# Kernel optimization log

Hardware: AMD Instinct MI355X
Metric: run time of the kernel (lower is better)

Reference implementation:

```python
import jax, jax.numpy as jnp
import numpy as np

NUM_GRAPHS = 64
NEG_SLOPE = 0.2


def _gatv2_layer(x, src, dst, edge_attr, Wl, Wr, We, att, b):
    """PyG GATv2Conv (heads=1) with self-loops (fill_value='mean')."""
    n = x.shape[0]
    # self-loop edge_attr = mean of incoming edge_attr per target node
    ones = jnp.ones((src.shape[0],), dtype=x.dtype)
    deg = jax.ops.segment_sum(ones, dst, num_segments=n)
    ea_sum = jax.ops.segment_sum(edge_attr, dst, num_segments=n)
    loop_attr = ea_sum / jnp.maximum(deg, 1.0)[:, None]
    loop = jnp.arange(n)
    src_f = jnp.concatenate([src, loop])
    dst_f = jnp.concatenate([dst, loop])
    ea_f = jnp.concatenate([edge_attr, loop_attr], axis=0)

    xl = x @ Wl              # source transform [N, out]
    xr = x @ Wr              # target transform [N, out]
    ee = ea_f @ We           # edge transform   [E+N, out]

    m = xl[src_f] + xr[dst_f] + ee                      # [E+N, out]
    m = jax.nn.leaky_relu(m, NEG_SLOPE)
    s = m @ att                                         # [E+N] attention logits

    # segment softmax over incoming edges of each target node
    smax = jax.ops.segment_max(s, dst_f, num_segments=n)
    e = jnp.exp(s - smax[dst_f])
    denom = jax.ops.segment_sum(e, dst_f, num_segments=n)
    alpha = e / (denom[dst_f] + 1e-16)

    out = jax.ops.segment_sum(alpha[:, None] * xl[src_f], dst_f, num_segments=n)
    return out + b


def setup_inputs() -> dict:
    key = jax.random.key(0)
    ks = jax.random.split(key, 16)
    N, E, D, ED = 50000, 640000, 128, 16
    sc = 0.1
    inp = {
        "node_features": jax.random.normal(ks[0], (N, D), jnp.float32),
        "edge_index": jax.random.randint(ks[1], (2, E), 0, N, jnp.int64),
        "batch": jnp.sort(jax.random.randint(ks[2], (N,), 0, 64, jnp.int64)),
        "edge_attr": jax.random.normal(ks[3], (E, ED), jnp.float32),
        "Wl1": jax.random.normal(ks[4], (D, D), jnp.float32) * sc,
        "Wr1": jax.random.normal(ks[5], (D, D), jnp.float32) * sc,
        "We1": jax.random.normal(ks[6], (ED, D), jnp.float32) * sc,
        "att1": jax.random.normal(ks[7], (D,), jnp.float32) * sc,
        "b1": jnp.zeros((D,), jnp.float32),
        "Wl2": jax.random.normal(ks[8], (D, D), jnp.float32) * sc,
        "Wr2": jax.random.normal(ks[9], (D, D), jnp.float32) * sc,
        "We2": jax.random.normal(ks[10], (ED, D), jnp.float32) * sc,
        "att2": jax.random.normal(ks[11], (D,), jnp.float32) * sc,
        "b2": jnp.zeros((D,), jnp.float32),
    }
    return inp


def reference(node_features, edge_index, batch, edge_attr,
              Wl1, Wr1, We1, att1, b1, Wl2, Wr2, We2, att2, b2):
    src, dst = edge_index[0], edge_index[1]
    x = _gatv2_layer(node_features, src, dst, edge_attr, Wl1, Wr1, We1, att1, b1)
    x = jax.nn.relu(x)
    x = _gatv2_layer(x, src, dst, edge_attr, Wl2, Wr2, We2, att2, b2)
    x = jax.nn.relu(x)
    # global mean pool over the full node set (node_subset_indices defaults to arange)
    cnt = jax.ops.segment_sum(jnp.ones((x.shape[0],), x.dtype), batch, num_segments=NUM_GRAPHS)
    pooled = jax.ops.segment_sum(x, batch, num_segments=NUM_GRAPHS)
    return pooled / jnp.maximum(cnt, 1.0)[:, None]
```

## Files before the change

### kernel.cpp

```cpp
#include <hip/hip_runtime.h>
#include <hip/hip_bf16.h>
#include <math.h>

#define D 128
#define ED 16
#define NUM_GRAPHS 64
#define SCAN_CHUNK 2048


__global__ void deg_kernel(const int* __restrict__ dst, int* __restrict__ deg, int E) {
  int e = blockIdx.x * 256 + threadIdx.x;
  if (e < E) atomicAdd(&deg[dst[e]], 1);
}

__global__ __launch_bounds__(256) void scan_reduce_kernel(const int* __restrict__ deg,
                                                          int* __restrict__ bsum, int N) {
  int b = blockIdx.x, tid = threadIdx.x;
  int base = b * SCAN_CHUNK + tid * 8;
  int s = 0;
#pragma unroll
  for (int j = 0; j < 8; ++j) {
    int idx = base + j;
    if (idx < N) s += deg[idx];
  }
#pragma unroll
  for (int off = 1; off < 64; off <<= 1) s += __shfl_xor(s, off);
  __shared__ int ws[4];
  int lane = tid & 63, w = tid >> 6;
  if (lane == 0) ws[w] = s;
  __syncthreads();
  if (tid == 0) bsum[b] = ws[0] + ws[1] + ws[2] + ws[3];
}

__global__ void scan_bsum_kernel(const int* __restrict__ bsum, int* __restrict__ boff,
                                 int* __restrict__ rowptrN, int B) {
  int tid = threadIdx.x;
  int v = (tid < B) ? bsum[tid] : 0;
  int x = v;
#pragma unroll
  for (int off = 1; off < 64; off <<= 1) {
    int y = __shfl_up(x, off);
    if (tid >= off) x += y;
  }
  if (tid < B) boff[tid] = x - v;
  if (tid == 63) *rowptrN = x;
}

__global__ __launch_bounds__(256) void scan_write_kernel(const int* __restrict__ deg,
                                                         const int* __restrict__ boff,
                                                         int* __restrict__ rowptr, int N) {
  int b = blockIdx.x, tid = threadIdx.x;
  int lane = tid & 63, w = tid >> 6;
  int base = b * SCAN_CHUNK + tid * 8;
  int v[8];
  int s = 0;
#pragma unroll
  for (int j = 0; j < 8; ++j) {
    int idx = base + j;
    v[j] = (idx < N) ? deg[idx] : 0;
    s += v[j];
  }
  int t = s, x = t;
#pragma unroll
  for (int off = 1; off < 64; off <<= 1) {
    int y = __shfl_up(x, off);
    if (lane >= off) x += y;
  }
  __shared__ int wsum[4];
  if (lane == 63) wsum[w] = x;
  __syncthreads();
  int wexc = 0;
  for (int i = 0; i < w; ++i) wexc += wsum[i];
  int run = boff[b] + wexc + (x - t);
#pragma unroll
  for (int j = 0; j < 8; ++j) {
    int idx = base + j;
    if (idx < N) rowptr[idx] = run;
    run += v[j];
  }
}

__global__ void scatter_kernel(const int* __restrict__ src, const int* __restrict__ dst,
                               const int* __restrict__ rowptr, int* __restrict__ cursor,
                               int2* __restrict__ csr, int E) {
  int e = blockIdx.x * 256 + threadIdx.x;
  if (e >= E) return;
  int d = dst[e];
  int pos = rowptr[d] + atomicAdd(&cursor[d], 1);
  csr[pos] = make_int2(src[e], e);
}

__global__ __launch_bounds__(256) void loopattr_kernel(const float* __restrict__ ea,
                                                       const int* __restrict__ rowptr,
                                                       const int2* __restrict__ csr,
                                                       float* __restrict__ ea_mean, int N) {
  int lane = threadIdx.x & 63;
  int wid = threadIdx.x >> 6;
  int n = blockIdx.x * 4 + wid;
  if (n >= N) return;
  int k = lane & 15, g = lane >> 4;
  int beg = rowptr[n], end = rowptr[n + 1];
  float s = 0.f;
  for (int i = beg + g; i < end; i += 4) {
    int eid = csr[i].y;
    s += ea[(size_t)eid * ED + k];
  }
  s += __shfl_xor(s, 16);
  s += __shfl_xor(s, 32);
  if (g == 0) ea_mean[(size_t)n * ED + k] = s / fmaxf((float)(end - beg), 1.0f);
}


__global__ __launch_bounds__(256) void gemm2_kernel(const float* __restrict__ x,
                                                    const float* __restrict__ Wl,
                                                    const float* __restrict__ Wr,
                                                    float* __restrict__ xl,
                                                    float* __restrict__ xr, int N) {
  __shared__ float xst[D][64];
  __shared__ float ws[16][256];
  int tid = threadIdx.x;
  int base = blockIdx.x * 64;

#pragma unroll
  for (int j = 0; j < 8; ++j) {
    int idx = tid + j * 256;
    int row = idx & 63;
    int c4 = idx >> 6;
    int n = base + row;
    float4 v = make_float4(0.f, 0.f, 0.f, 0.f);
    if (n < N) v = *(const float4*)&x[(size_t)n * D + c4 * 4];
    xst[c4 * 4 + 0][row] = v.x;
    xst[c4 * 4 + 1][row] = v.y;
    xst[c4 * 4 + 2][row] = v.z;
    xst[c4 * 4 + 3][row] = v.w;
  }

  int tn = tid & 15;
  int tc = tid >> 4;
  float acc[4][16];
#pragma unroll
  for (int i = 0; i < 4; ++i)
#pragma unroll
    for (int j = 0; j < 16; ++j) acc[i][j] = 0.f;

  for (int kb = 0; kb < D; kb += 16) {
    __syncthreads();
#pragma unroll
    for (int j = 0; j < 4; ++j) {
      int idx = tid + j * 256;
      int c4 = idx & 63;
      int kk = idx >> 6;
      int c = c4 * 4;
      const float* Wp = (c < D) ? &Wl[(size_t)(kb + kk) * D + c]
                                : &Wr[(size_t)(kb + kk) * D + (c - D)];
      *(float4*)&ws[kk][c] = *(const float4*)Wp;
    }
    __syncthreads();
#pragma unroll
    for (int kk = 0; kk < 16; ++kk) {
      float4 xv = *(float4*)&xst[kb + kk][tn * 4];
      float xa[4] = {xv.x, xv.y, xv.z, xv.w};
      float4 w0 = *(float4*)&ws[kk][tc * 16 + 0];
      float4 w1 = *(float4*)&ws[kk][tc * 16 + 4];
      float4 w2 = *(float4*)&ws[kk][tc * 16 + 8];
      float4 w3 = *(float4*)&ws[kk][tc * 16 + 12];
      float wa[16] = {w0.x, w0.y, w0.z, w0.w, w1.x, w1.y, w1.z, w1.w,
                      w2.x, w2.y, w2.z, w2.w, w3.x, w3.y, w3.z, w3.w};
#pragma unroll
      for (int i = 0; i < 4; ++i)
#pragma unroll
        for (int j = 0; j < 16; ++j) acc[i][j] = fmaf(xa[i], wa[j], acc[i][j]);
    }
  }

#pragma unroll
  for (int i = 0; i < 4; ++i) {
    int n = base + tn * 4 + i;
    if (n >= N) continue;
    float* outp;
    int c;
    if (tc < 8) { outp = xl; c = tc * 16; }
    else        { outp = xr; c = (tc - 8) * 16; }
#pragma unroll
    for (int j4 = 0; j4 < 4; ++j4) {
      float4 v = make_float4(acc[i][j4 * 4 + 0], acc[i][j4 * 4 + 1],
                             acc[i][j4 * 4 + 2], acc[i][j4 * 4 + 3]);
      *(float4*)&outp[(size_t)n * D + c + j4 * 4] = v;
    }
  }
}


__global__ __launch_bounds__(256) void gat_fused_kernel(
    const float* __restrict__ xl, const float* __restrict__ xr,
    const int* __restrict__ rowptr, const int2* __restrict__ csr,
    const float* __restrict__ ea, const float* __restrict__ ea_mean,
    const float* __restrict__ We, const float* __restrict__ att,
    const float* __restrict__ bias, float* __restrict__ y, int N) {
  __shared__ float ea_lds[4][4][16];
  int lane = threadIdx.x & 63;
  int wid = threadIdx.x >> 6;
  int n = blockIdx.x * 4 + wid;
  if (n >= N) return;

  float weL[ED], weH[ED];
#pragma unroll
  for (int k = 0; k < ED; ++k) {
    float2 w = *(const float2*)&We[k * D + 2 * lane];
    weL[k] = w.x;
    weH[k] = w.y;
  }
  float2 xrv = *(const float2*)&xr[(size_t)n * D + 2 * lane];
  float2 attv = *(const float2*)&att[2 * lane];
  float2 bv = *(const float2*)&bias[2 * lane];

  int beg = rowptr[n], end = rowptr[n + 1];

  float denom, acc0, acc1;
  {
    float2 xsl = *(const float2*)&xl[(size_t)n * D + 2 * lane];
    const float4* ap = (const float4*)&ea_mean[(size_t)n * ED];
    float4 q0 = ap[0], q1 = ap[1], q2 = ap[2], q3 = ap[3];
    float av[16] = {q0.x, q0.y, q0.z, q0.w, q1.x, q1.y, q1.z, q1.w,
                    q2.x, q2.y, q2.z, q2.w, q3.x, q3.y, q3.z, q3.w};
    float e0 = 0.f, e1 = 0.f;
#pragma unroll
    for (int k = 0; k < ED; ++k) {
      e0 = fmaf(av[k], weL[k], e0);
      e1 = fmaf(av[k], weH[k], e1);
    }
    float t0 = xsl.x + xrv.x + e0;
    t0 = (t0 > 0.f) ? t0 : 0.2f * t0;
    float t1 = xsl.y + xrv.y + e1;
    t1 = (t1 > 0.f) ? t1 : 0.2f * t1;
    float p = fmaf(t0, attv.x, t1 * attv.y);
#pragma unroll
    for (int off = 32; off > 0; off >>= 1) p += __shfl_xor(p, off);
    float w = __expf(p);
    denom = w;
    acc0 = w * xsl.x;
    acc1 = w * xsl.y;
  }

  int ej = lane >> 4;
  int ek = lane & 15;

  for (int i = beg; i < end; i += 4) {
    int cnt = end - i;
    int last = end - 1;
    int i1 = (i + 1 < end) ? i + 1 : last;
    int i2 = (i + 2 < end) ? i + 2 : last;
    int i3 = (i + 3 < end) ? i + 3 : last;
    int2 c0 = csr[i], c1 = csr[i1], c2 = csr[i2], c3 = csr[i3];

    float2 xs0 = *(const float2*)&xl[(size_t)c0.x * D + 2 * lane];
    float2 xs1 = *(const float2*)&xl[(size_t)c1.x * D + 2 * lane];
    float2 xs2 = *(const float2*)&xl[(size_t)c2.x * D + 2 * lane];
    float2 xs3 = *(const float2*)&xl[(size_t)c3.x * D + 2 * lane];

    int eidj = (ej == 0) ? c0.y : (ej == 1) ? c1.y : (ej == 2) ? c2.y : c3.y;
    float a = ea[(size_t)eidj * ED + ek];
    ea_lds[wid][ej][ek] = a;

    float pre[4];
    float2 xsa[4] = {xs0, xs1, xs2, xs3};
#pragma unroll
    for (int j = 0; j < 4; ++j) {
      const float4* eap = (const float4*)&ea_lds[wid][j][0];
      float4 q0 = eap[0], q1 = eap[1], q2 = eap[2], q3 = eap[3];
      float av[16] = {q0.x, q0.y, q0.z, q0.w, q1.x, q1.y, q1.z, q1.w,
                      q2.x, q2.y, q2.z, q2.w, q3.x, q3.y, q3.z, q3.w};
      float e0 = 0.f, e1 = 0.f;
#pragma unroll
      for (int k = 0; k < ED; ++k) {
        e0 = fmaf(av[k], weL[k], e0);
        e1 = fmaf(av[k], weH[k], e1);
      }
      float t0 = xsa[j].x + xrv.x + e0;
      t0 = (t0 > 0.f) ? t0 : 0.2f * t0;
      float t1 = xsa[j].y + xrv.y + e1;
      t1 = (t1 > 0.f) ? t1 : 0.2f * t1;
      pre[j] = fmaf(t0, attv.x, t1 * attv.y);
    }

#pragma unroll
    for (int off = 32; off > 0; off >>= 1) {
#pragma unroll
      for (int j = 0; j < 4; ++j) pre[j] += __shfl_xor(pre[j], off);
    }

#pragma unroll
    for (int j = 0; j < 4; ++j) {
      float w = (j < cnt) ? __expf(pre[j]) : 0.f;
      denom += w;
      acc0 = fmaf(w, xsa[j].x, acc0);
      acc1 = fmaf(w, xsa[j].y, acc1);
    }
  }

  float inv = 1.0f / (denom + 1e-16f);
  float o0 = fmaxf(fmaf(acc0, inv, bv.x), 0.f);
  float o1 = fmaxf(fmaf(acc1, inv, bv.y), 0.f);
  *(float2*)&y[(size_t)n * D + 2 * lane] = make_float2(o0, o1);
}


__global__ __launch_bounds__(128) void pool_kernel(const float* __restrict__ y,
                                                   const int* __restrict__ batch,
                                                   float* __restrict__ out, int N) {
  int g = blockIdx.x;
  int part = blockIdx.y;
  int d = threadIdx.x;
  __shared__ int se[2];
  if (d < 2) {
    int target = g + d;
    int lo = 0, hi = N;
    while (lo < hi) {
      int mid = (lo + hi) >> 1;
      if (batch[mid] < target) lo = mid + 1;
      else hi = mid;
    }
    se[d] = lo;
  }
  __syncthreads();
  int start = se[0], end = se[1];
  int len = end - start;
  int q = (len + 3) >> 2;
  int ps = start + part * q;
  int pe = min(ps + q, end);
  float s0 = 0.f, s1 = 0.f, s2 = 0.f, s3 = 0.f;
  int nn = ps;
  for (; nn + 3 < pe; nn += 4) {
    s0 += y[(size_t)(nn + 0) * D + d];
    s1 += y[(size_t)(nn + 1) * D + d];
    s2 += y[(size_t)(nn + 2) * D + d];
    s3 += y[(size_t)(nn + 3) * D + d];
  }
  for (; nn < pe; ++nn) s0 += y[(size_t)nn * D + d];
  float sum = (s0 + s1) + (s2 + s3);
  float cnt = fmaxf((float)len, 1.0f);
  if (ps < pe) atomicAdd(&out[g * D + d], sum / cnt);
  else if (part == 0 && len <= 0) out[g * D + d] = 0.f;
}


static inline size_t alignup(size_t v) { return (v + 255) & ~(size_t)255; }

extern "C" void kernel_launch(void* const* d_in, const int* in_sizes, int n_in,
                              void* d_out, int out_size, void* d_ws, size_t ws_size,
                              hipStream_t stream) {
  const float* xnode = (const float*)d_in[0];
  const int* eidx = (const int*)d_in[1];
  const int* batch = (const int*)d_in[2];
  const float* eattr = (const float*)d_in[3];
  const float* Wl1 = (const float*)d_in[4];
  const float* Wr1 = (const float*)d_in[5];
  const float* We1 = (const float*)d_in[6];
  const float* att1 = (const float*)d_in[7];
  const float* b1 = (const float*)d_in[8];
  const float* Wl2 = (const float*)d_in[9];
  const float* Wr2 = (const float*)d_in[10];
  const float* We2 = (const float*)d_in[11];
  const float* att2 = (const float*)d_in[12];
  const float* b2 = (const float*)d_in[13];
  float* out = (float*)d_out;

  int N = in_sizes[0] / D;
  int E = in_sizes[3] / ED;
  const int* srcp = eidx;
  const int* dstp = eidx + E;
  int B = (N + SCAN_CHUNK - 1) / SCAN_CHUNK;

  char* p = (char*)d_ws;
  int* rowptr = (int*)p;    p += alignup((size_t)(N + 1) * 4);
  int* deg = (int*)p;       p += alignup((size_t)N * 4);
  int* cursor = (int*)p;    p += alignup((size_t)N * 4);
  int* bsum = (int*)p;      p += alignup((size_t)B * 4);
  int* boff = (int*)p;      p += alignup((size_t)B * 4);
  int2* csr = (int2*)p;     p += alignup((size_t)E * 8);
  float* ea_mean = (float*)p; p += alignup((size_t)N * ED * 4);
  float* xlb = (float*)p;   p += alignup((size_t)N * D * 4);
  float* xrb = (float*)p;   p += alignup((size_t)N * D * 4);
  float* yb = (float*)p;    p += alignup((size_t)N * D * 4);

  hipMemsetAsync(deg, 0, (size_t)N * 4, stream);
  hipMemsetAsync(cursor, 0, (size_t)N * 4, stream);
  hipMemsetAsync(out, 0, (size_t)NUM_GRAPHS * D * 4, stream);

  deg_kernel<<<(E + 255) / 256, 256, 0, stream>>>(dstp, deg, E);
  scan_reduce_kernel<<<B, 256, 0, stream>>>(deg, bsum, N);
  scan_bsum_kernel<<<1, 64, 0, stream>>>(bsum, boff, rowptr + N, B);
  scan_write_kernel<<<B, 256, 0, stream>>>(deg, boff, rowptr, N);
  scatter_kernel<<<(E + 255) / 256, 256, 0, stream>>>(srcp, dstp, rowptr, cursor, csr, E);
  loopattr_kernel<<<(N + 3) / 4, 256, 0, stream>>>(eattr, rowptr, csr, ea_mean, N);

  int agrid = (N + 3) / 4;

  gemm2_kernel<<<(N + 63) / 64, 256, 0, stream>>>(xnode, Wl1, Wr1, xlb, xrb, N);
  gat_fused_kernel<<<agrid, 256, 0, stream>>>(xlb, xrb, rowptr, csr, eattr, ea_mean,
                                              We1, att1, b1, yb, N);
  gemm2_kernel<<<(N + 63) / 64, 256, 0, stream>>>(yb, Wl2, Wr2, xlb, xrb, N);
  gat_fused_kernel<<<agrid, 256, 0, stream>>>(xlb, xrb, rowptr, csr, eattr, ea_mean,
                                              We2, att2, b2, yb, N);
  dim3 pgrid(NUM_GRAPHS, 4);
  pool_kernel<<<pgrid, 128, 0, stream>>>(yb, batch, out, N);

  (void)ws_size; (void)n_in; (void)out_size;
}
```

Before: 652.0 us.

## Fuse self-loop edge-attr mean into GAT kernel and use persistent grid-stride waves

Removes the separate loopattr kernel and its ea_mean buffer by accumulating the incoming edge_attr sum inside the GAT aggregation loop. The self-loop term is then computed after the neighbour loop rather than before it. The GAT kernel also switches to a fixed grid of 2048 blocks whose waves walk the nodes with a grid stride, which amortises the We register loads across many nodes. In exchange the mean is recomputed in both layers, and a fixed grid size may balance load worse across nodes with uneven degrees.

```diff
diff --git a/kernel.cpp b/kernel.cpp
--- a/kernel.cpp
+++ b/kernel.cpp
@@ -88,26 +88,6 @@
   int d = dst[e];
   int pos = rowptr[d] + atomicAdd(&cursor[d], 1);
   csr[pos] = make_int2(src[e], e);
-}
-
-__global__ __launch_bounds__(256) void loopattr_kernel(const float* __restrict__ ea,
-                                                       const int* __restrict__ rowptr,
-                                                       const int2* __restrict__ csr,
-                                                       float* __restrict__ ea_mean, int N) {
-  int lane = threadIdx.x & 63;
-  int wid = threadIdx.x >> 6;
-  int n = blockIdx.x * 4 + wid;
-  if (n >= N) return;
-  int k = lane & 15, g = lane >> 4;
-  int beg = rowptr[n], end = rowptr[n + 1];
-  float s = 0.f;
-  for (int i = beg + g; i < end; i += 4) {
-    int eid = csr[i].y;
-    s += ea[(size_t)eid * ED + k];
-  }
-  s += __shfl_xor(s, 16);
-  s += __shfl_xor(s, 32);
-  if (g == 0) ea_mean[(size_t)n * ED + k] = s / fmaxf((float)(end - beg), 1.0f);
 }
 
 
@@ -194,14 +174,13 @@
 __global__ __launch_bounds__(256) void gat_fused_kernel(
     const float* __restrict__ xl, const float* __restrict__ xr,
     const int* __restrict__ rowptr, const int2* __restrict__ csr,
-    const float* __restrict__ ea, const float* __restrict__ ea_mean,
-    const float* __restrict__ We, const float* __restrict__ att,
-    const float* __restrict__ bias, float* __restrict__ y, int N) {
+    const float* __restrict__ ea, const float* __restrict__ We,
+    const float* __restrict__ att, const float* __restrict__ bias,
+    float* __restrict__ y, int N, int nwaves) {
   __shared__ float ea_lds[4][4][16];
   int lane = threadIdx.x & 63;
   int wid = threadIdx.x >> 6;
-  int n = blockIdx.x * 4 + wid;
-  if (n >= N) return;
+  int gwave = blockIdx.x * 4 + wid;
 
   float weL[ED], weH[ED];
 #pragma unroll
@@ -210,63 +189,79 @@
     weL[k] = w.x;
     weH[k] = w.y;
   }
-  float2 xrv = *(const float2*)&xr[(size_t)n * D + 2 * lane];
   float2 attv = *(const float2*)&att[2 * lane];
   float2 bv = *(const float2*)&bias[2 * lane];
 
-  int beg = rowptr[n], end = rowptr[n + 1];
-
-  float denom, acc0, acc1;
-  {
-    float2 xsl = *(const float2*)&xl[(size_t)n * D + 2 * lane];
-    const float4* ap = (const float4*)&ea_mean[(size_t)n * ED];
-    float4 q0 = ap[0], q1 = ap[1], q2 = ap[2], q3 = ap[3];
-    float av[16] = {q0.x, q0.y, q0.z, q0.w, q1.x, q1.y, q1.z, q1.w,
-                    q2.x, q2.y, q2.z, q2.w, q3.x, q3.y, q3.z, q3.w};
-    float e0 = 0.f, e1 = 0.f;
-#pragma unroll
-    for (int k = 0; k < ED; ++k) {
-      e0 = fmaf(av[k], weL[k], e0);
-      e1 = fmaf(av[k], weH[k], e1);
-    }
-    float t0 = xsl.x + xrv.x + e0;
-    t0 = (t0 > 0.f) ? t0 : 0.2f * t0;
-    float t1 = xsl.y + xrv.y + e1;
-    t1 = (t1 > 0.f) ? t1 : 0.2f * t1;
-    float p = fmaf(t0, attv.x, t1 * attv.y);
-#pragma unroll
-    for (int off = 32; off > 0; off >>= 1) p += __shfl_xor(p, off);
-    float w = __expf(p);
-    denom = w;
-    acc0 = w * xsl.x;
-    acc1 = w * xsl.y;
-  }
-
   int ej = lane >> 4;
   int ek = lane & 15;
 
-  for (int i = beg; i < end; i += 4) {
-    int cnt = end - i;
-    int last = end - 1;
-    int i1 = (i + 1 < end) ? i + 1 : last;
-    int i2 = (i + 2 < end) ? i + 2 : last;
-    int i3 = (i + 3 < end) ? i + 3 : last;
-    int2 c0 = csr[i], c1 = csr[i1], c2 = csr[i2], c3 = csr[i3];
-
-    float2 xs0 = *(const float2*)&xl[(size_t)c0.x * D + 2 * lane];
-    float2 xs1 = *(const float2*)&xl[(size_t)c1.x * D + 2 * lane];
-    float2 xs2 = *(const float2*)&xl[(size_t)c2.x * D + 2 * lane];
-    float2 xs3 = *(const float2*)&xl[(size_t)c3.x * D + 2 * lane];
-
-    int eidj = (ej == 0) ? c0.y : (ej == 1) ? c1.y : (ej == 2) ? c2.y : c3.y;
-    float a = ea[(size_t)eidj * ED + ek];
-    ea_lds[wid][ej][ek] = a;
-
-    float pre[4];
-    float2 xsa[4] = {xs0, xs1, xs2, xs3};
-#pragma unroll
-    for (int j = 0; j < 4; ++j) {
-      const float4* eap = (const float4*)&ea_lds[wid][j][0];
+  for (int n = gwave; n < N; n += nwaves) {
+    float2 xrv = *(const float2*)&xr[(size_t)n * D + 2 * lane];
+    float2 xsl = *(const float2*)&xl[(size_t)n * D + 2 * lane];
+    int beg = rowptr[n], end = rowptr[n + 1];
+
+    float denom = 0.f, acc0 = 0.f, acc1 = 0.f, easum = 0.f;
+
+    for (int i = beg; i < end; i += 4) {
+      int cnt = end - i;
+      int last = end - 1;
+      int i1 = (i + 1 < end) ? i + 1 : last;
+      int i2 = (i + 2 < end) ? i + 2 : last;
+      int i3 = (i + 3 < end) ? i + 3 : last;
+      int2 c0 = csr[i], c1 = csr[i1], c2 = csr[i2], c3 = csr[i3];
+
+      float2 xs0 = *(const float2*)&xl[(size_t)c0.x * D + 2 * lane];
+      float2 xs1 = *(const float2*)&xl[(size_t)c1.x * D + 2 * lane];
+      float2 xs2 = *(const float2*)&xl[(size_t)c2.x * D + 2 * lane];
+      float2 xs3 = *(const float2*)&xl[(size_t)c3.x * D + 2 * lane];
+
+      int eidj = (ej == 0) ? c0.y : (ej == 1) ? c1.y : (ej == 2) ? c2.y : c3.y;
+      float a = ea[(size_t)eidj * ED + ek];
+      ea_lds[wid][ej][ek] = a;
+      easum += (ej < cnt) ? a : 0.f;
+
+      float pre[4];
+      float2 xsa[4] = {xs0, xs1, xs2, xs3};
+#pragma unroll
+      for (int j = 0; j < 4; ++j) {
+        const float4* eap = (const float4*)&ea_lds[wid][j][0];
+        float4 q0 = eap[0], q1 = eap[1], q2 = eap[2], q3 = eap[3];
+        float av[16] = {q0.x, q0.y, q0.z, q0.w, q1.x, q1.y, q1.z, q1.w,
+                        q2.x, q2.y, q2.z, q2.w, q3.x, q3.y, q3.z, q3.w};
+        float e0 = 0.f, e1 = 0.f;
+#pragma unroll
+        for (int k = 0; k < ED; ++k) {
+          e0 = fmaf(av[k], weL[k], e0);
+          e1 = fmaf(av[k], weH[k], e1);
+        }
+        float t0 = xsa[j].x + xrv.x + e0;
+        t0 = (t0 > 0.f) ? t0 : 0.2f * t0;
+        float t1 = xsa[j].y + xrv.y + e1;
+        t1 = (t1 > 0.f) ? t1 : 0.2f * t1;
+        pre[j] = fmaf(t0, attv.x, t1 * attv.y);
+      }
+
+#pragma unroll
+      for (int off = 32; off > 0; off >>= 1) {
+#pragma unroll
+        for (int j = 0; j < 4; ++j) pre[j] += __shfl_xor(pre[j], off);
+      }
+
+#pragma unroll
+      for (int j = 0; j < 4; ++j) {
+        float w = (j < cnt) ? __expf(pre[j]) : 0.f;
+        denom += w;
+        acc0 = fmaf(w, xsa[j].x, acc0);
+        acc1 = fmaf(w, xsa[j].y, acc1);
+      }
+    }
+
+    easum += __shfl_xor(easum, 16);
+    easum += __shfl_xor(easum, 32);
+    float dg = fmaxf((float)(end - beg), 1.0f);
+    if (ej == 0) ea_lds[wid][0][ek] = easum / dg;
+    {
+      const float4* eap = (const float4*)&ea_lds[wid][0][0];
       float4 q0 = eap[0], q1 = eap[1], q2 = eap[2], q3 = eap[3];
       float av[16] = {q0.x, q0.y, q0.z, q0.w, q1.x, q1.y, q1.z, q1.w,
                       q2.x, q2.y, q2.z, q2.w, q3.x, q3.y, q3.z, q3.w};
@@ -276,32 +271,24 @@
         e0 = fmaf(av[k], weL[k], e0);
         e1 = fmaf(av[k], weH[k], e1);
       }
-      float t0 = xsa[j].x + xrv.x + e0;
+      float t0 = xsl.x + xrv.x + e0;
       t0 = (t0 > 0.f) ? t0 : 0.2f * t0;
-      float t1 = xsa[j].y + xrv.y + e1;
+      float t1 = xsl.y + xrv.y + e1;
       t1 = (t1 > 0.f) ? t1 : 0.2f * t1;
-      pre[j] = fmaf(t0, attv.x, t1 * attv.y);
-    }
-
-#pragma unroll
-    for (int off = 32; off > 0; off >>= 1) {
-#pragma unroll
-      for (int j = 0; j < 4; ++j) pre[j] += __shfl_xor(pre[j], off);
-    }
-
-#pragma unroll
-    for (int j = 0; j < 4; ++j) {
-      float w = (j < cnt) ? __expf(pre[j]) : 0.f;
+      float p = fmaf(t0, attv.x, t1 * attv.y);
+#pragma unroll
+      for (int off = 32; off > 0; off >>= 1) p += __shfl_xor(p, off);
+      float w = __expf(p);
       denom += w;
-      acc0 = fmaf(w, xsa[j].x, acc0);
-      acc1 = fmaf(w, xsa[j].y, acc1);
-    }
-  }
-
-  float inv = 1.0f / (denom + 1e-16f);
-  float o0 = fmaxf(fmaf(acc0, inv, bv.x), 0.f);
-  float o1 = fmaxf(fmaf(acc1, inv, bv.y), 0.f);
-  *(float2*)&y[(size_t)n * D + 2 * lane] = make_float2(o0, o1);
+      acc0 = fmaf(w, xsl.x, acc0);
+      acc1 = fmaf(w, xsl.y, acc1);
+    }
+
+    float inv = 1.0f / (denom + 1e-16f);
+    float o0 = fmaxf(fmaf(acc0, inv, bv.x), 0.f);
+    float o1 = fmaxf(fmaf(acc1, inv, bv.y), 0.f);
+    *(float2*)&y[(size_t)n * D + 2 * lane] = make_float2(o0, o1);
+  }
 }
 
 
@@ -378,7 +365,6 @@
   int* bsum = (int*)p;      p += alignup((size_t)B * 4);
   int* boff = (int*)p;      p += alignup((size_t)B * 4);
   int2* csr = (int2*)p;     p += alignup((size_t)E * 8);
-  float* ea_mean = (float*)p; p += alignup((size_t)N * ED * 4);
   float* xlb = (float*)p;   p += alignup((size_t)N * D * 4);
   float* xrb = (float*)p;   p += alignup((size_t)N * D * 4);
   float* yb = (float*)p;    p += alignup((size_t)N * D * 4);
@@ -392,16 +378,16 @@
   scan_bsum_kernel<<<1, 64, 0, stream>>>(bsum, boff, rowptr + N, B);
   scan_write_kernel<<<B, 256, 0, stream>>>(deg, boff, rowptr, N);
   scatter_kernel<<<(E + 255) / 256, 256, 0, stream>>>(srcp, dstp, rowptr, cursor, csr, E);
-  loopattr_kernel<<<(N + 3) / 4, 256, 0, stream>>>(eattr, rowptr, csr, ea_mean, N);
-
-  int agrid = (N + 3) / 4;
+
+  int gblocks = 2048;
+  int nwaves = gblocks * 4;
 
   gemm2_kernel<<<(N + 63) / 64, 256, 0, stream>>>(xnode, Wl1, Wr1, xlb, xrb, N);
-  gat_fused_kernel<<<agrid, 256, 0, stream>>>(xlb, xrb, rowptr, csr, eattr, ea_mean,
-                                              We1, att1, b1, yb, N);
+  gat_fused_kernel<<<gblocks, 256, 0, stream>>>(xlb, xrb, rowptr, csr, eattr,
+                                                We1, att1, b1, yb, N, nwaves);
   gemm2_kernel<<<(N + 63) / 64, 256, 0, stream>>>(yb, Wl2, Wr2, xlb, xrb, N);
-  gat_fused_kernel<<<agrid, 256, 0, stream>>>(xlb, xrb, rowptr, csr, eattr, ea_mean,
-                                              We2, att2, b2, yb, N);
+  gat_fused_kernel<<<gblocks, 256, 0, stream>>>(xlb, xrb, rowptr, csr, eattr,
+                                                We2, att2, b2, yb, N, nwaves);
   dim3 pgrid(NUM_GRAPHS, 4);
   pool_kernel<<<pgrid, 128, 0, stream>>>(yb, batch, out, N);
 
```

Result: faster. 610.9 us (-6.3%).
